# Performance work log

Hardware: AMD Instinct MI355X
Metric: run time of the kernel (lower is better)

The kernel has to match this reference:

```python
import jax, jax.numpy as jnp
import numpy as np

EPS = 1e-12  # torch F.normalize eps
NUM_HEADS = 4
DT = 0.25
NUM_STEPS = 4


def _l2norm(x, axis=-1):
    n = jnp.sqrt(jnp.sum(x * x, axis=axis, keepdims=True))
    return x / jnp.maximum(n, EPS)


def setup_inputs() -> dict:
    key = jax.random.key(0)
    k0, k1, k2, k3, k4 = jax.random.split(key, 5)
    B, T, D = 4, 2048, 256
    z = jax.random.normal(k0, (B, T, D), dtype=jnp.float32)
    omega = jax.random.normal(k1, (1, 1, D), dtype=jnp.float32) * 0.1
    Wqk = jax.random.normal(k2, (2 * D, D), dtype=jnp.float32) * (1.0 / np.sqrt(D))
    Wout = jax.random.normal(k3, (D, D), dtype=jnp.float32) * (1.0 / np.sqrt(D))
    bout = jax.random.normal(k4, (D,), dtype=jnp.float32) * 0.01
    return {"z": z, "omega": omega, "Wqk": Wqk, "Wout": Wout, "bout": bout}


def _kuramoto(x, omega, Wqk, Wout, bout):
    # x: [B, T, D]
    B, T, D = x.shape
    hd = D // NUM_HEADS
    qk = x @ Wqk.T  # [B, T, 2D]
    q, k = jnp.split(qk, 2, axis=-1)
    q = _l2norm(q.reshape(B, T, NUM_HEADS, hd))  # cosine-normalized per head
    k = _l2norm(k.reshape(B, T, NUM_HEADS, hd))
    # coupling: [B, H, T, T] cosine similarity
    coupling = jnp.einsum("bqhd,bkhd->bhqk", q, k)
    # sin nonlinearity replaces softmax
    force = jnp.einsum("bhqk,bkhd->bqhd", jnp.sin(coupling), k).reshape(B, T, D)
    return omega + force @ Wout.T + bout


def reference(z, omega, Wqk, Wout, bout):
    def f(x):
        return _kuramoto(x, omega, Wqk, Wout, bout)

    x = z
    for _ in range(NUM_STEPS):
        x = _l2norm(x)
        k1 = f(x)
        k2 = f(x + DT / 2 * k1)
        k3 = f(x + DT / 2 * k2)
        k4 = f(x + DT * k3)
        x = x + DT / 6 * (k1 + 2 * k2 + 2 * k3 + k4)
    return _l2norm(x)
```

## Files before the change

kernel.cpp:

```cpp
#include <hip/hip_runtime.h>
#include <cmath>

#define NB 4
#define TT 2048
#define DD 256
#define NH 4
#define BT (NB*TT)

static constexpr float DT_ = 0.25f;

typedef _Float16 f16x8 __attribute__((ext_vector_type(8)));
typedef _Float16 f16x4 __attribute__((ext_vector_type(4)));
typedef float    f32x4 __attribute__((ext_vector_type(4)));
typedef float    f32x16 __attribute__((ext_vector_type(16)));

static constexpr size_t HSZ = (size_t)NB * NH * TT * 64;
static constexpr size_t FSZ = (size_t)BT * 256;

__device__ __forceinline__ void gload16(const void* g, void* l) {
    __builtin_amdgcn_global_load_lds(
        (const __attribute__((address_space(1))) void*)g,
        (__attribute__((address_space(3))) void*)l,
        16, 0, 0);
}

__global__ __launch_bounds__(256)
void split_weights(const float* __restrict__ Wqk, const float* __restrict__ Wout,
                   _Float16* __restrict__ WqkH, _Float16* __restrict__ WqkL,
                   _Float16* __restrict__ WoutH, _Float16* __restrict__ WoutL)
{
    const int idx = blockIdx.x * 256 + threadIdx.x;
    const float4 v = (idx < 32768) ? ((const float4*)Wqk)[idx]
                                   : ((const float4*)Wout)[idx - 32768];
    f16x4 h, l;
    h[0]=(_Float16)v.x; l[0]=(_Float16)(v.x-(float)h[0]);
    h[1]=(_Float16)v.y; l[1]=(_Float16)(v.y-(float)h[1]);
    h[2]=(_Float16)v.z; l[2]=(_Float16)(v.z-(float)h[2]);
    h[3]=(_Float16)v.w; l[3]=(_Float16)(v.w-(float)h[3]);
    if (idx < 32768) { ((f16x4*)WqkH)[idx] = h; ((f16x4*)WqkL)[idx] = l; }
    else { ((f16x4*)WoutH)[idx-32768] = h; ((f16x4*)WoutL)[idx-32768] = l; }
}

__global__ __launch_bounds__(256)
void comb_weights(const float* __restrict__ Wqk, const float* __restrict__ Wout,
                  const float* __restrict__ omega, const float* __restrict__ bout,
                  _Float16* __restrict__ WcombH, _Float16* __restrict__ WcombL,
                  float* __restrict__ qkob)
{
    __shared__ float qrow[256];
    __shared__ float pr[256];
    const int n = blockIdx.x;
    const int k = threadIdx.x;
    qrow[k] = Wqk[n * 256 + k];
    __syncthreads();
    float s = 0.f;
    for (int m = 0; m < 256; ++m) s = fmaf(qrow[m], Wout[m * 256 + k], s);
    const _Float16 h = (_Float16)s;
    WcombH[n * 256 + k] = h;
    WcombL[n * 256 + k] = (_Float16)(s - (float)h);
    pr[k] = (omega[k] + bout[k]) * qrow[k];
    __syncthreads();
    if (k == 0) {
        float t = 0.f;
        for (int i = 0; i < 256; ++i) t += pr[i];
        qkob[n] = t;
    }
}

__global__ __launch_bounds__(256)
void l2norm_rows(const float* __restrict__ src, float* __restrict__ dst,
                 _Float16* __restrict__ dstH, _Float16* __restrict__ dstL) {
    const int wave = threadIdx.x >> 6;
    const int lane = threadIdx.x & 63;
    const size_t row = (size_t)blockIdx.x * 4 + wave;
    float4 v = ((const float4*)(src + row * DD))[lane];
    float ss = v.x*v.x + v.y*v.y + v.z*v.z + v.w*v.w;
    #pragma unroll
    for (int off = 32; off; off >>= 1) ss += __shfl_xor(ss, off, 64);
    const float inv = 1.0f / fmaxf(sqrtf(ss), 1e-12f);
    v.x *= inv; v.y *= inv; v.z *= inv; v.w *= inv;
    ((float4*)(dst + row * DD))[lane] = v;
    if (dstH != nullptr) {
        f16x4 h, l;
        h[0]=(_Float16)v.x; l[0]=(_Float16)(v.x-(float)h[0]);
        h[1]=(_Float16)v.y; l[1]=(_Float16)(v.y-(float)h[1]);
        h[2]=(_Float16)v.z; l[2]=(_Float16)(v.z-(float)h[2]);
        h[3]=(_Float16)v.w; l[3]=(_Float16)(v.w-(float)h[3]);
        ((f16x4*)(dstH + row * DD))[lane] = h;
        ((f16x4*)(dstL + row * DD))[lane] = l;
    }
}

__global__ __launch_bounds__(256, 2)
void gemm_mfma(const _Float16* __restrict__ AH, const _Float16* __restrict__ AL,
               const _Float16* __restrict__ BH, const _Float16* __restrict__ BL,
               const float* __restrict__ Fp, float* __restrict__ FaccP,
               float* __restrict__ qkx, const float* __restrict__ qkob,
               const float* __restrict__ omega, const float* __restrict__ bout,
               const float* __restrict__ xin, float* __restrict__ xout,
               _Float16* __restrict__ Qhi, _Float16* __restrict__ Qlo,
               _Float16* __restrict__ Khi, _Float16* __restrict__ Klo,
               _Float16* __restrict__ KtrH,
               int mode, float cc, int faccm)
{
    __shared__ _Float16 Ah[128 * 64];
    __shared__ _Float16 Al[128 * 64];
    __shared__ _Float16 Bh[64 * 64];
    __shared__ _Float16 Bl[64 * 64];
    const int m0 = blockIdx.x * 128, n0 = blockIdx.y * 64;
    const int t  = threadIdx.x;
    const int w  = t >> 6;
    const int l  = t & 63;
    const int lr = l & 15;
    const int lq = l >> 4;
    const int m7 = lr & 7;
    const int rr = l >> 3;
    const int lc  = l & 7;
    const int cg  = (lc ^ rr) * 8;
    const int swd = (lc ^ rr) * 8;
    const bool yzero = (blockIdx.y == 0);

    f32x4 acc[2][4];
    #pragma unroll
    for (int s = 0; s < 2; ++s)
        #pragma unroll
        for (int nt = 0; nt < 4; ++nt) acc[s][nt] = (f32x4){0.f,0.f,0.f,0.f};

#define GSTAGE_A(K0) do { \
        _Pragma("unroll") \
        for (int a = 0; a < 4; ++a) { \
            const int rg = 8*w + 32*a; \
            gload16(AH + (size_t)(m0 + rg + rr) * 256 + (K0) + cg, &Ah[rg * 64]); \
            gload16(AL + (size_t)(m0 + rg + rr) * 256 + (K0) + cg, &Al[rg * 64]); \
        } \
    } while (0)

#define GSTAGE_B(K0) do { \
        _Pragma("unroll") \
        for (int a = 0; a < 2; ++a) { \
            const int rg = 8*w + 32*a; \
            gload16(BH + (size_t)(n0 + rg + rr) * 256 + (K0) + cg, &Bh[rg * 64]); \
            gload16(BL + (size_t)(n0 + rg + rr) * 256 + (K0) + cg, &Bl[rg * 64]); \
        } \
    } while (0)

#define FSTAGE(K0) do { \
        _Pragma("unroll") \
        for (int a = 0; a < 4; ++a) { \
            const int row = 8*w + 32*a + rr; \
            const size_t go = (size_t)(m0 + row) * 256 + (K0) + lc * 8; \
            float sv[8]; \
            { const float4 a0 = *(const float4*)(Fp + go); \
              const float4 a1 = *(const float4*)(Fp + go + 4); \
              sv[0]=a0.x; sv[1]=a0.y; sv[2]=a0.z; sv[3]=a0.w; \
              sv[4]=a1.x; sv[5]=a1.y; sv[6]=a1.z; sv[7]=a1.w; } \
            _Pragma("unroll") \
            for (int p = 1; p < 3; ++p) { \
                const float4 a0 = *(const float4*)(Fp + (size_t)p*FSZ + go); \
                const float4 a1 = *(const float4*)(Fp + (size_t)p*FSZ + go + 4); \
                sv[0]+=a0.x; sv[1]+=a0.y; sv[2]+=a0.z; sv[3]+=a0.w; \
                sv[4]+=a1.x; sv[5]+=a1.y; sv[6]+=a1.z; sv[7]+=a1.w; } \
            if (faccm == 3) { \
                const float4 f0 = *(const float4*)(FaccP + go); \
                const float4 f1 = *(const float4*)(FaccP + go + 4); \
                sv[0]+=f0.x; sv[1]+=f0.y; sv[2]+=f0.z; sv[3]+=f0.w; \
                sv[4]+=f1.x; sv[5]+=f1.y; sv[6]+=f1.z; sv[7]+=f1.w; \
            } else if (yzero) { \
                if (faccm == 1) { \
                    *(float4*)(FaccP + go)     = make_float4(sv[0], sv[1], sv[2], sv[3]); \
                    *(float4*)(FaccP + go + 4) = make_float4(sv[4], sv[5], sv[6], sv[7]); \
                } else { \
                    float4 f0 = *(const float4*)(FaccP + go); \
                    float4 f1 = *(const float4*)(FaccP + go + 4); \
                    f0.x += 2.f*sv[0]; f0.y += 2.f*sv[1]; f0.z += 2.f*sv[2]; f0.w += 2.f*sv[3]; \
                    f1.x += 2.f*sv[4]; f1.y += 2.f*sv[5]; f1.z += 2.f*sv[6]; f1.w += 2.f*sv[7]; \
                    *(float4*)(FaccP + go)     = f0; \
                    *(float4*)(FaccP + go + 4) = f1; \
                } \
            } \
            f16x8 hv, lv; \
            _Pragma("unroll") \
            for (int e = 0; e < 8; ++e) { \
                hv[e] = (_Float16)sv[e]; \
                lv[e] = (_Float16)(sv[e] - (float)hv[e]); } \
            *(f16x8*)&Ah[row * 64 + swd] = hv; \
            *(f16x8*)&Al[row * 64 + swd] = lv; \
        } \
    } while (0)

    if (mode == 0) GSTAGE_A(0); else FSTAGE(0);
    GSTAGE_B(0);
    asm volatile("s_waitcnt vmcnt(0) lgkmcnt(0)" ::: "memory");
    __builtin_amdgcn_s_barrier();
    asm volatile("" ::: "memory");

    for (int kc = 0; kc < 4; ++kc) {
        f16x8 ah[2][2], al[2][2], bh[2][4], bl[2][4];
        #pragma unroll
        for (int c = 0; c < 2; ++c) {
            const int xo = (((4*c + lq) ^ m7) << 4);
            #pragma unroll
            for (int s = 0; s < 2; ++s) {
                ah[c][s] = *(const f16x8*)((const char*)Ah + (32*w + 16*s + lr) * 128 + xo);
                al[c][s] = *(const f16x8*)((const char*)Al + (32*w + 16*s + lr) * 128 + xo);
            }
            #pragma unroll
            for (int nt = 0; nt < 4; ++nt) {
                bh[c][nt] = *(const f16x8*)((const char*)Bh + (16*nt + lr) * 128 + xo);
                bl[c][nt] = *(const f16x8*)((const char*)Bl + (16*nt + lr) * 128 + xo);
            }
        }
        asm volatile("s_waitcnt lgkmcnt(0)" ::: "memory");
        __builtin_amdgcn_s_barrier();
        asm volatile("" ::: "memory");
        if (kc < 3) {
            GSTAGE_B((kc + 1) * 64);
            if (mode == 0) GSTAGE_A((kc + 1) * 64); else FSTAGE((kc + 1) * 64);
        }
        #pragma unroll
        for (int c = 0; c < 2; ++c)
            #pragma unroll
            for (int s = 0; s < 2; ++s)
                #pragma unroll
                for (int nt = 0; nt < 4; ++nt) {
                    acc[s][nt] = __builtin_amdgcn_mfma_f32_16x16x32_f16(ah[c][s], bh[c][nt], acc[s][nt], 0, 0, 0);
                    acc[s][nt] = __builtin_amdgcn_mfma_f32_16x16x32_f16(ah[c][s], bl[c][nt], acc[s][nt], 0, 0, 0);
                    acc[s][nt] = __builtin_amdgcn_mfma_f32_16x16x32_f16(al[c][s], bh[c][nt], acc[s][nt], 0, 0, 0);
                }
        if (kc < 3) asm volatile("s_waitcnt vmcnt(0) lgkmcnt(0)" ::: "memory");
        __builtin_amdgcn_s_barrier();
        asm volatile("" ::: "memory");
    }
#undef GSTAGE_A
#undef GSTAGE_B
#undef FSTAGE

    if (mode == 2) {
        #pragma unroll
        for (int s = 0; s < 2; ++s) {
            const int row0 = m0 + 32*w + 16*s + 4*lq;
            #pragma unroll
            for (int nt = 0; nt < 4; ++nt) {
                const int col = n0 + 16*nt + lr;
                const float ob = omega[col] + bout[col];
                #pragma unroll
                for (int r = 0; r < 4; ++r) {
                    const size_t off = (size_t)(row0 + r) * 256 + col;
                    xout[off] = xin[off] + (DT_ / 6.0f) * acc[s][nt][r] + DT_ * ob;
                }
            }
        }
    } else {
        float val[2][4][4];
        #pragma unroll
        for (int s = 0; s < 2; ++s) {
            const int row0 = m0 + 32*w + 16*s + 4*lq;
            #pragma unroll
            for (int nt = 0; nt < 4; ++nt) {
                const int col = n0 + 16*nt + lr;
                #pragma unroll
                for (int r = 0; r < 4; ++r) {
                    const size_t qo = (size_t)(row0 + r) * 512 + col;
                    if (mode == 0) {
                        val[s][nt][r] = acc[s][nt][r];
                        qkx[qo] = acc[s][nt][r];
                    } else {
                        val[s][nt][r] = qkx[qo] + cc * (acc[s][nt][r] + qkob[col]);
                    }
                }
            }
        }
        float ss[2][4];
        #pragma unroll
        for (int s = 0; s < 2; ++s)
            #pragma unroll
            for (int r = 0; r < 4; ++r) {
                float v = 0.f;
                #pragma unroll
                for (int nt = 0; nt < 4; ++nt) v += val[s][nt][r] * val[s][nt][r];
                ss[s][r] = v;
            }
        #pragma unroll
        for (int off = 1; off < 16; off <<= 1)
            #pragma unroll
            for (int s = 0; s < 2; ++s)
                #pragma unroll
                for (int r = 0; r < 4; ++r)
                    ss[s][r] += __shfl_xor(ss[s][r], off, 64);
        const int  b    = m0 >> 11;
        const int  h    = (n0 >> 6) & 3;
        const bool is_k = (n0 >= 256);
        const size_t bhi = (size_t)b * NH + h;
        _Float16* dhi = (is_k ? Khi : Qhi) + bhi * (size_t)TT * 64;
        _Float16* dlo = (is_k ? Klo : Qlo) + bhi * (size_t)TT * 64;
        const int mloc = m0 & (TT - 1);
        _Float16* Pt = Ah;
        #pragma unroll
        for (int s = 0; s < 2; ++s) {
            const int r0 = 32*w + 16*s + 4*lq;
            float inv[4];
            #pragma unroll
            for (int r = 0; r < 4; ++r) inv[r] = 1.0f / fmaxf(sqrtf(ss[s][r]), 1e-12f);
            #pragma unroll
            for (int nt = 0; nt < 4; ++nt) {
                const int d = 16*nt + lr;
                f16x4 hv, lv;
                #pragma unroll
                for (int r = 0; r < 4; ++r) {
                    const float v2 = val[s][nt][r] * inv[r];
                    hv[r] = (_Float16)v2;
                    lv[r] = (_Float16)(v2 - (float)hv[r]);
                    dhi[(size_t)(mloc + r0 + r) * 64 + d] = hv[r];
                    dlo[(size_t)(mloc + r0 + r) * 64 + d] = lv[r];
                }
                if (is_k) {
                    *(f16x4*)((char*)Pt + d * 256 + ((r0 * 2) ^ ((d & 7) << 4))) = hv;
                }
            }
        }
        if (is_k) {
            __syncthreads();
            const size_t kb = bhi * (size_t)64 * TT + mloc;
            #pragma unroll
            for (int p = 0; p < 4; ++p) {
                const int d   = (t >> 4) + 16 * p;
                const int lm0 = (t & 15) * 8;
                f16x8 v = *(const f16x8*)((const char*)Pt + d * 256 + ((lm0 * 2) ^ ((d & 7) << 4)));
                *(f16x8*)(KtrH + kb + (size_t)d * TT + lm0) = v;
            }
        }
    }
}

__global__ __launch_bounds__(256, 3)
void kuramoto_attn(const _Float16* __restrict__ Qhi, const _Float16* __restrict__ Qlo,
                   const _Float16* __restrict__ Khi, const _Float16* __restrict__ Klo,
                   const _Float16* __restrict__ KtrH,
                   float* __restrict__ Fp)
{
    __shared__ _Float16 KjH[64 * 64];
    __shared__ _Float16 KjL[64 * 64];
    __shared__ _Float16 KdH[64 * 64];
    const int bh = blockIdx.x;
    const int b  = bh >> 2, h = bh & 3;
    const size_t base  = (size_t)bh * TT * 64;
    const size_t tbase = (size_t)bh * 64 * TT;
    const int t0 = blockIdx.y * 11;
    const int tn = (blockIdx.y == 2) ? 10 : 11;
    float* Fout = Fp + (size_t)blockIdx.y * FSZ;
    const int t = threadIdx.x;
    const int w = t >> 6;
    const int l = t & 63;
    const int il = l & 31;
    const int h5 = l >> 5;
    const int i0 = blockIdx.z * 128 + w * 32;
    const int s7 = il & 7;
    const int rr = l >> 3;
    const int lc8 = (l & 7) * 8;
    const int sw = ((l & 7) ^ rr) * 8;
    const int rg = 8 * w + rr;

    f16x8 qh[4], ql[4];
    #pragma unroll
    for (int kc = 0; kc < 4; ++kc) {
        const size_t qoff = base + (size_t)(i0 + il) * 64 + 16*kc + 8*h5;
        qh[kc] = *(const f16x8*)(Qhi + qoff);
        ql[kc] = *(const f16x8*)(Qlo + qoff);
    }

    f32x16 Fac[2];
    #pragma unroll
    for (int db = 0; db < 2; ++db)
        #pragma unroll
        for (int r = 0; r < 16; ++r) Fac[db][r] = 0.f;

    uint4 gA0, gA1, gB0, gB1, gC0, gC1;
#define GLOAD(TTi) do { \
        const int j0_ = (t0 + (TTi)) * 64; \
        gA0 = *(const uint4*)(Khi  + base  + (size_t)(j0_ + rg)      * 64 + lc8); \
        gA1 = *(const uint4*)(Khi  + base  + (size_t)(j0_ + rg + 32) * 64 + lc8); \
        gB0 = *(const uint4*)(Klo  + base  + (size_t)(j0_ + rg)      * 64 + lc8); \
        gB1 = *(const uint4*)(Klo  + base  + (size_t)(j0_ + rg + 32) * 64 + lc8); \
        gC0 = *(const uint4*)(KtrH + tbase + (size_t)rg        * TT + j0_ + lc8); \
        gC1 = *(const uint4*)(KtrH + tbase + (size_t)(rg + 32) * TT + j0_ + lc8); \
    } while (0)

    GLOAD(0);

    for (int tt = 0; tt < tn; ++tt) {
        *(uint4*)&KjH[rg * 64 + sw]        = gA0;
        *(uint4*)&KjH[(rg + 32) * 64 + sw] = gA1;
        *(uint4*)&KjL[rg * 64 + sw]        = gB0;
        *(uint4*)&KjL[(rg + 32) * 64 + sw] = gB1;
        *(uint4*)&KdH[rg * 64 + sw]        = gC0;
        *(uint4*)&KdH[(rg + 32) * 64 + sw] = gC1;
        if (tt + 1 < tn) GLOAD(tt + 1);
        asm volatile("s_waitcnt lgkmcnt(0)" ::: "memory");
        __builtin_amdgcn_s_barrier();
        asm volatile("" ::: "memory");

        f16x8 ph[2][2];
        #pragma unroll
        for (int jb = 0; jb < 2; ++jb) {
            f32x16 sacc;
            #pragma unroll
            for (int r = 0; r < 16; ++r) sacc[r] = 0.f;
            const int rowb = (32*jb + il) * 128;
            __builtin_amdgcn_s_setprio(1);
            #pragma unroll
            for (int kc = 0; kc < 4; ++kc) {
                const int ch = (((2*kc + h5) ^ s7) << 4);
                f16x8 khA = *(const f16x8*)((const char*)KjH + rowb + ch);
                f16x8 klA = *(const f16x8*)((const char*)KjL + rowb + ch);
                sacc = __builtin_amdgcn_mfma_f32_32x32x16_f16(khA, qh[kc], sacc, 0, 0, 0);
                sacc = __builtin_amdgcn_mfma_f32_32x32x16_f16(klA, qh[kc], sacc, 0, 0, 0);
                sacc = __builtin_amdgcn_mfma_f32_32x32x16_f16(khA, ql[kc], sacc, 0, 0, 0);
            }
            __builtin_amdgcn_s_setprio(0);
            f16x8 v0, v1;
            #pragma unroll
            for (int e = 0; e < 8; ++e) {
                v0[e] = (_Float16)__sinf(sacc[e]);
                v1[e] = (_Float16)__sinf(sacc[8 + e]);
            }
            ph[jb][0] = v0;
            ph[jb][1] = v1;
        }

        #pragma unroll
        for (int db = 0; db < 2; ++db) {
            const int rowd = (il + 32*db) * 128;
            __builtin_amdgcn_s_setprio(1);
            #pragma unroll
            for (int jb = 0; jb < 2; ++jb)
                #pragma unroll
                for (int cp = 0; cp < 2; ++cp) {
                    const int q1 = 4*jb + 2*cp;
                    f16x4 klo = *(const f16x4*)((const char*)KdH + rowd + ((q1 ^ s7) << 4) + 8*h5);
                    f16x4 khi = *(const f16x4*)((const char*)KdH + rowd + (((q1 + 1) ^ s7) << 4) + 8*h5);
                    f16x8 kf;
                    #pragma unroll
                    for (int e = 0; e < 4; ++e) { kf[e] = klo[e]; kf[4 + e] = khi[e]; }
                    Fac[db] = __builtin_amdgcn_mfma_f32_32x32x16_f16(ph[jb][cp], kf, Fac[db], 0, 0, 0);
                }
            __builtin_amdgcn_s_setprio(0);
        }
        __builtin_amdgcn_s_barrier();
        asm volatile("" ::: "memory");
    }
#undef GLOAD

    #pragma unroll
    for (int db = 0; db < 2; ++db)
        #pragma unroll
        for (int r = 0; r < 16; ++r) {
            const int irow = (r & 3) + 8 * (r >> 2) + 4 * h5;
            Fout[((size_t)b * TT + i0 + irow) * 256 + h * 64 + il + 32 * db] = Fac[db][r];
        }
}

extern "C" void kernel_launch(void* const* d_in, const int* in_sizes, int n_in,
                              void* d_out, int out_size, void* d_ws, size_t ws_size,
                              hipStream_t stream) {
    const float* z     = (const float*)d_in[0];
    const float* omega = (const float*)d_in[1];
    const float* Wqk   = (const float*)d_in[2];
    const float* Wout  = (const float*)d_in[3];
    const float* bout  = (const float*)d_in[4];

    float* x    = (float*)d_ws;
    float* Facc = x + FSZ;
    float* Fp   = Facc + FSZ;
    float* qkx  = Fp + 3 * FSZ;
    float* qkob = qkx + (size_t)BT * 512;
    _Float16* xsH  = (_Float16*)(qkob + 512);
    _Float16* xsL  = xsH  + FSZ;
    _Float16* Qhi  = xsL  + FSZ;
    _Float16* Qlo  = Qhi  + HSZ;
    _Float16* Khi  = Qlo  + HSZ;
    _Float16* Klo  = Khi  + HSZ;
    _Float16* KtrH = Klo  + HSZ;
    _Float16* WqkH = KtrH + HSZ;
    _Float16* WqkL = WqkH + (size_t)512 * 256;
    _Float16* WoutH= WqkL + (size_t)512 * 256;
    _Float16* WoutL= WoutH + (size_t)256 * 256;
    _Float16* WcombH = WoutL + (size_t)256 * 256;
    _Float16* WcombL = WcombH + (size_t)512 * 256;

    split_weights<<<192, 256, 0, stream>>>(Wqk, Wout, WqkH, WqkL, WoutH, WoutL);
    comb_weights<<<512, 256, 0, stream>>>(Wqk, Wout, omega, bout, WcombH, WcombL, qkob);

    for (int step = 0; step < 4; ++step) {
        l2norm_rows<<<BT / 4, 256, 0, stream>>>(step == 0 ? z : x, x, xsH, xsL);
        gemm_mfma<<<dim3(BT / 128, 8), 256, 0, stream>>>(
            xsH, xsL, WqkH, WqkL, nullptr, nullptr, qkx, nullptr,
            nullptr, nullptr, nullptr, nullptr,
            Qhi, Qlo, Khi, Klo, KtrH, 0, 0.f, 0);
        kuramoto_attn<<<dim3(NB * NH, 3, TT / 128), 256, 0, stream>>>(
            Qhi, Qlo, Khi, Klo, KtrH, Fp);
        for (int s = 1; s <= 3; ++s) {
            const float cs = (s == 3) ? 0.25f : 0.125f;
            gemm_mfma<<<dim3(BT / 128, 8), 256, 0, stream>>>(
                nullptr, nullptr, WcombH, WcombL, Fp, Facc, qkx, qkob,
                nullptr, nullptr, nullptr, nullptr,
                Qhi, Qlo, Khi, Klo, KtrH, 1, cs, (s == 1) ? 1 : 2);
            kuramoto_attn<<<dim3(NB * NH, 3, TT / 128), 256, 0, stream>>>(
                Qhi, Qlo, Khi, Klo, KtrH, Fp);
        }
        gemm_mfma<<<dim3(BT / 128, 4), 256, 0, stream>>>(
            nullptr, nullptr, WoutH, WoutL, Fp, Facc, nullptr, nullptr,
            omega, bout, x, x,
            nullptr, nullptr, nullptr, nullptr, nullptr, 2, 0.f, 3);
    }
    l2norm_rows<<<BT / 4, 256, 0, stream>>>(x, (float*)d_out, nullptr, nullptr);
}
```

Baseline: 1.170 ms.

## Load K tiles via direct global-to-LDS and pre-permute transposed K layout

Replaces the register-staged, software-prefetched K tile loads with global_load_lds direct-to-LDS transfers, waited on with vmcnt and bracketed by __syncthreads. The transposed-K writer now permutes 4-element groups so the PV MFMA can read one f16x8 per operand instead of two f16x4 halves plus a repack. The QK accumulation is split into two independent accumulators to shorten the MFMA dependency chain. The cost is losing the next-tile prefetch overlap, since each tile load is now waited on synchronously.

Measured after the change: 1.184 ms. Within noise of the previous version (+1.2%).

```diff
diff --git a/kernel.cpp b/kernel.cpp
--- a/kernel.cpp
+++ b/kernel.cpp
@@ -324,9 +324,16 @@
             #pragma unroll
             for (int p = 0; p < 4; ++p) {
                 const int d   = (t >> 4) + 16 * p;
-                const int lm0 = (t & 15) * 8;
-                f16x8 v = *(const f16x8*)((const char*)Pt + d * 256 + ((lm0 * 2) ^ ((d & 7) << 4)));
-                *(f16x8*)(KtrH + kb + (size_t)d * TT + lm0) = v;
+                const int g   = t & 15;
+                const int win = g >> 3, gw = g & 7;
+                const int Ga  = 16*win + 4*(gw >> 1) + (gw & 1);
+                const int Gb  = Ga + 2;
+                f16x4 va = *(const f16x4*)((const char*)Pt + d * 256 + ((8*Ga) ^ ((d & 7) << 4)));
+                f16x4 vb = *(const f16x4*)((const char*)Pt + d * 256 + ((8*Gb) ^ ((d & 7) << 4)));
+                f16x8 v;
+                #pragma unroll
+                for (int e = 0; e < 4; ++e) { v[e] = va[e]; v[4 + e] = vb[e]; }
+                *(f16x8*)(KtrH + kb + (size_t)d * TT + 8*g) = v;
             }
         }
     }
@@ -356,9 +363,7 @@
     const int i0 = blockIdx.z * 128 + w * 32;
     const int s7 = il & 7;
     const int rr = l >> 3;
-    const int lc8 = (l & 7) * 8;
-    const int sw = ((l & 7) ^ rr) * 8;
-    const int rg = 8 * w + rr;
+    const int cg = ((l & 7) ^ rr) * 8;
 
     f16x8 qh[4], ql[4];
     #pragma unroll
@@ -374,37 +379,24 @@
         #pragma unroll
         for (int r = 0; r < 16; ++r) Fac[db][r] = 0.f;
 
-    uint4 gA0, gA1, gB0, gB1, gC0, gC1;
-#define GLOAD(TTi) do { \
-        const int j0_ = (t0 + (TTi)) * 64; \
-        gA0 = *(const uint4*)(Khi  + base  + (size_t)(j0_ + rg)      * 64 + lc8); \
-        gA1 = *(const uint4*)(Khi  + base  + (size_t)(j0_ + rg + 32) * 64 + lc8); \
-        gB0 = *(const uint4*)(Klo  + base  + (size_t)(j0_ + rg)      * 64 + lc8); \
-        gB1 = *(const uint4*)(Klo  + base  + (size_t)(j0_ + rg + 32) * 64 + lc8); \
-        gC0 = *(const uint4*)(KtrH + tbase + (size_t)rg        * TT + j0_ + lc8); \
-        gC1 = *(const uint4*)(KtrH + tbase + (size_t)(rg + 32) * TT + j0_ + lc8); \
-    } while (0)
-
-    GLOAD(0);
-
     for (int tt = 0; tt < tn; ++tt) {
-        *(uint4*)&KjH[rg * 64 + sw]        = gA0;
-        *(uint4*)&KjH[(rg + 32) * 64 + sw] = gA1;
-        *(uint4*)&KjL[rg * 64 + sw]        = gB0;
-        *(uint4*)&KjL[(rg + 32) * 64 + sw] = gB1;
-        *(uint4*)&KdH[rg * 64 + sw]        = gC0;
-        *(uint4*)&KdH[(rg + 32) * 64 + sw] = gC1;
-        if (tt + 1 < tn) GLOAD(tt + 1);
-        asm volatile("s_waitcnt lgkmcnt(0)" ::: "memory");
-        __builtin_amdgcn_s_barrier();
-        asm volatile("" ::: "memory");
+        const int j0 = (t0 + tt) * 64;
+        __syncthreads();
+        gload16(Khi + base + (size_t)(j0 + 8*w + rr) * 64 + cg,       &KjH[(8*w) * 64]);
+        gload16(Khi + base + (size_t)(j0 + 8*w + rr + 32) * 64 + cg,  &KjH[(8*w + 32) * 64]);
+        gload16(Klo + base + (size_t)(j0 + 8*w + rr) * 64 + cg,       &KjL[(8*w) * 64]);
+        gload16(Klo + base + (size_t)(j0 + 8*w + rr + 32) * 64 + cg,  &KjL[(8*w + 32) * 64]);
+        gload16(KtrH + tbase + (size_t)(8*w + rr) * TT + j0 + cg,     &KdH[(8*w) * 64]);
+        gload16(KtrH + tbase + (size_t)(8*w + rr + 32) * TT + j0 + cg,&KdH[(8*w + 32) * 64]);
+        asm volatile("s_waitcnt vmcnt(0)" ::: "memory");
+        __syncthreads();
 
         f16x8 ph[2][2];
         #pragma unroll
         for (int jb = 0; jb < 2; ++jb) {
-            f32x16 sacc;
-            #pragma unroll
-            for (int r = 0; r < 16; ++r) sacc[r] = 0.f;
+            f32x16 sA, sB;
+            #pragma unroll
+            for (int r = 0; r < 16; ++r) { sA[r] = 0.f; sB[r] = 0.f; }
             const int rowb = (32*jb + il) * 128;
             __builtin_amdgcn_s_setprio(1);
             #pragma unroll
@@ -412,16 +404,16 @@
                 const int ch = (((2*kc + h5) ^ s7) << 4);
                 f16x8 khA = *(const f16x8*)((const char*)KjH + rowb + ch);
                 f16x8 klA = *(const f16x8*)((const char*)KjL + rowb + ch);
-                sacc = __builtin_amdgcn_mfma_f32_32x32x16_f16(khA, qh[kc], sacc, 0, 0, 0);
-                sacc = __builtin_amdgcn_mfma_f32_32x32x16_f16(klA, qh[kc], sacc, 0, 0, 0);
-                sacc = __builtin_amdgcn_mfma_f32_32x32x16_f16(khA, ql[kc], sacc, 0, 0, 0);
+                sA = __builtin_amdgcn_mfma_f32_32x32x16_f16(khA, qh[kc], sA, 0, 0, 0);
+                sB = __builtin_amdgcn_mfma_f32_32x32x16_f16(klA, qh[kc], sB, 0, 0, 0);
+                sB = __builtin_amdgcn_mfma_f32_32x32x16_f16(khA, ql[kc], sB, 0, 0, 0);
             }
             __builtin_amdgcn_s_setprio(0);
             f16x8 v0, v1;
             #pragma unroll
             for (int e = 0; e < 8; ++e) {
-                v0[e] = (_Float16)__sinf(sacc[e]);
-                v1[e] = (_Float16)__sinf(sacc[8 + e]);
+                v0[e] = (_Float16)__sinf(sA[e] + sB[e]);
+                v1[e] = (_Float16)__sinf(sA[8 + e] + sB[8 + e]);
             }
             ph[jb][0] = v0;
             ph[jb][1] = v1;
@@ -432,23 +424,13 @@
             const int rowd = (il + 32*db) * 128;
             __builtin_amdgcn_s_setprio(1);
             #pragma unroll
-            for (int jb = 0; jb < 2; ++jb)
-                #pragma unroll
-                for (int cp = 0; cp < 2; ++cp) {
-                    const int q1 = 4*jb + 2*cp;
-                    f16x4 klo = *(const f16x4*)((const char*)KdH + rowd + ((q1 ^ s7) << 4) + 8*h5);
-                    f16x4 khi = *(const f16x4*)((const char*)KdH + rowd + (((q1 + 1) ^ s7) << 4) + 8*h5);
-                    f16x8 kf;
-                    #pragma unroll
-                    for (int e = 0; e < 4; ++e) { kf[e] = klo[e]; kf[4 + e] = khi[e]; }
-                    Fac[db] = __builtin_amdgcn_mfma_f32_32x32x16_f16(ph[jb][cp], kf, Fac[db], 0, 0, 0);
-                }
+            for (int cp = 0; cp < 4; ++cp) {
+                f16x8 kf = *(const f16x8*)((const char*)KdH + rowd + (((2*cp + h5) ^ s7) << 4));
+                Fac[db] = __builtin_amdgcn_mfma_f32_32x32x16_f16(ph[cp >> 1][cp & 1], kf, Fac[db], 0, 0, 0);
+            }
             __builtin_amdgcn_s_setprio(0);
         }
-        __builtin_amdgcn_s_barrier();
-        asm volatile("" ::: "memory");
-    }
-#undef GLOAD
+    }
 
     #pragma unroll
     for (int db = 0; db < 2; ++db)
```
